# Kernel tuning notes

Hardware: AMD Instinct MI355X
Metric: run time of the kernel (lower is better)

Reference implementation:

```python
import jax, jax.numpy as jnp
import numpy as np

B, L, R, D = 64, 512, 512, 512
F_CONV, H = 100, 60

def setup_inputs() -> dict:
    key = jax.random.key(0)
    ks = jax.random.split(key, 8)
    l_lengths = jax.random.randint(ks[0], (B,), L // 2, L + 1)
    r_lengths = jax.random.randint(ks[1], (B,), R // 2, R + 1)
    l_vectors = jax.random.normal(ks[2], (L, B, D), jnp.float32)
    r_vectors = jax.random.normal(ks[3], (R, B, D), jnp.float32)
    Wconv = jax.random.normal(ks[4], (F_CONV, D), jnp.float32) / np.sqrt(D).astype(np.float32)
    bconv = jnp.zeros((F_CONV,), jnp.float32)
    Wd = jax.random.normal(ks[5], (H, 2 * F_CONV), jnp.float32) / np.sqrt(2 * F_CONV).astype(np.float32)
    bd = jnp.zeros((H,), jnp.float32)
    return {"l_lengths": l_lengths, "l_vectors": l_vectors, "r_lengths": r_lengths,
            "r_vectors": r_vectors, "Wconv": Wconv, "bconv": bconv, "Wd": Wd, "bd": bd}

def reference(l_lengths, l_vectors, r_lengths, r_vectors, Wconv, bconv, Wd, bd):
    Lm, Bm, Dm = l_vectors.shape
    Rm = r_vectors.shape[0]
    # masks, seq-first [L,B] like pad_sequence output
    l_mask = (jnp.arange(Lm)[:, None] < l_lengths[None, :]).astype(l_vectors.dtype)
    r_mask = (jnp.arange(Rm)[:, None] < r_lengths[None, :]).astype(r_vectors.dtype)
    lmT, rmT = l_mask.T, r_mask.T  # [B,L], [B,R]

    # co-attention scores [B,L,R]
    attention = jnp.einsum('lbd,rbd->blr', l_vectors, r_vectors)
    attention = attention * lmT[:, :, None] * rmT[:, None, :]

    att_r = jax.nn.softmax(attention - 10.0 * (1.0 - lmT[:, :, None]), axis=1)
    att_r = att_r * lmT[:, :, None]
    att_r = att_r / (att_r.sum(axis=1, keepdims=True) + 1e-13)

    att_l = jax.nn.softmax(attention - 10.0 * (1.0 - rmT[:, None, :]), axis=2)
    att_l = att_l * rmT[:, None, :]
    att_l = att_l / (att_l.sum(axis=2, keepdims=True) + 1e-13)

    # ---- left side: stats + top-1 hard attention ----
    rl = r_lengths.astype(l_vectors.dtype)[:, None]
    l_mean = att_l.sum(axis=2) / rl                              # [B,L]
    l_w = (att_l * att_l).sum(axis=2) / rl - l_mean * l_mean
    l_w = l_w / jnp.maximum(l_mean, 0.001)
    l_a = att_l.max(axis=2)                                      # top-1 value [B,L]
    l_i = att_l.argmax(axis=2)                                   # top-1 index [B,L]
    l_i = l_i * lmT.astype(l_i.dtype)
    l_a = l_a / jnp.maximum(l_a, 0.001)                          # k=1: sum == value
    gathered = jnp.take_along_axis(r_vectors, l_i.T[:, :, None], axis=0)  # [L,B,D]
    l_counter = l_a.T[:, :, None] * gathered
    l_c = l_w.T[:, :, None] * jnp.abs(l_vectors - l_counter) * l_mask[:, :, None]

    # ---- right side ----
    ll = l_lengths.astype(r_vectors.dtype)[:, None]
    r_mean = att_r.sum(axis=1) / ll                              # [B,R]
    r_w = (att_r * att_r).sum(axis=1) / ll - r_mean * r_mean
    r_w = r_w / jnp.maximum(r_mean, 0.001)
    r_a = att_r.max(axis=1)                                      # [B,R]
    r_i = att_r.argmax(axis=1)
    r_i = r_i * rmT.astype(r_i.dtype)
    r_a = r_a / jnp.maximum(r_a, 0.001)
    gathered_r = jnp.take_along_axis(l_vectors, r_i.T[:, :, None], axis=0)  # [R,B,D]
    r_counter = r_a.T[:, :, None] * gathered_r
    r_c = r_w.T[:, :, None] * jnp.abs(r_vectors - r_counter) * r_mask[:, :, None]

    # SentenceConv(1, 100, dim): kernel (1, dim) conv == per-position linear,
    # ReLU, masked max-pool over the sequence.
    def sconv(x, mask):  # x [S,B,D], mask [S,B]
        h = jax.nn.relu(jnp.einsum('sbd,fd->bsf', x, Wconv) + bconv)  # [B,S,F]
        h = h - (1.0 - mask.T)[:, :, None] * 1e9
        return h.max(axis=1)  # [B,F]

    feats = jnp.concatenate([sconv(l_c, l_mask), sconv(r_c, r_mask)], axis=1)  # [B,200]
    return jax.nn.relu(feats @ Wd.T + bd)  # [B,60]
```

## Files before the change

### kernel.cpp

```cpp
#include <hip/hip_runtime.h>
#include <math.h>

#define BB 64
#define LL 512
#define RR 512
#define DD 512
#define FC 100
#define FP 112
#define HH 60
#define BD (BB*DD)

typedef __attribute__((ext_vector_type(8))) short bf16x8;
typedef __attribute__((ext_vector_type(4))) float f32x4;

__device__ __forceinline__ unsigned short bf16rne(float x) {
  unsigned u = __float_as_uint(x);
  return (unsigned short)((u + 0x7fffu + ((u >> 16) & 1u)) >> 16);
}
__device__ __forceinline__ float bf16tof(unsigned short h) {
  return __uint_as_float((unsigned)h << 16);
}

__device__ __forceinline__ void bar_lgkm() {
  asm volatile("s_waitcnt lgkmcnt(0)" ::: "memory");
  __builtin_amdgcn_s_barrier();
}

__device__ __forceinline__ void split2(float x0, float x1, unsigned& h2, unsigned& l2) {
  unsigned u0 = __float_as_uint(x0), u1 = __float_as_uint(x1);
  h2 = __builtin_amdgcn_perm(u1, u0, 0x07060302u);
  float r0 = x0 - __uint_as_float(u0 & 0xffff0000u);
  float r1 = x1 - __uint_as_float(u1 & 0xffff0000u);
  l2 = __builtin_amdgcn_perm(__float_as_uint(r1), __float_as_uint(r0), 0x07060302u);
}

template <int N>
__device__ __forceinline__ float ror_max_f(float v) {
  return fmaxf(v, __uint_as_float(__builtin_amdgcn_mov_dpp(__float_as_uint(v), 0x120 | N, 0xf, 0xf, true)));
}
template <int N>
__device__ __forceinline__ float ror_add_f(float v) {
  return v + __uint_as_float(__builtin_amdgcn_mov_dpp(__float_as_uint(v), 0x120 | N, 0xf, 0xf, true));
}
template <int N>
__device__ __forceinline__ int ror_min_i(int v) {
  int o = __builtin_amdgcn_mov_dpp(v, 0x120 | N, 0xf, 0xf, true);
  return o < v ? o : v;
}
__device__ __forceinline__ float row16_max(float v) {
  v = ror_max_f<1>(v); v = ror_max_f<2>(v); v = ror_max_f<4>(v); return ror_max_f<8>(v);
}
__device__ __forceinline__ float row16_sum(float v) {
  v = ror_add_f<1>(v); v = ror_add_f<2>(v); v = ror_add_f<4>(v); return ror_add_f<8>(v);
}
__device__ __forceinline__ int row16_min(int v) {
  v = ror_min_i<1>(v); v = ror_min_i<2>(v); v = ror_min_i<4>(v); return ror_min_i<8>(v);
}

__global__ __launch_bounds__(512, 2) void gemm_att(const float* __restrict__ lv,
                                                   const float* __restrict__ rv,
                                                   const int* __restrict__ llen,
                                                   const int* __restrict__ rlen,
                                                   float4* __restrict__ lpart,
                                                   float4* __restrict__ rpart) {
  __shared__ __align__(16) unsigned short Ah[2][256][32];
  __shared__ __align__(16) unsigned short Al[2][256][32];
  __shared__ __align__(16) unsigned short Bh[2][256][32];
  __shared__ __align__(16) unsigned short Bl[2][256][32];

  const int bid = blockIdx.x;
  const int wid = (bid & 7) * 32 + (bid >> 3);
  const int b  = wid >> 2;
  const int l0 = ((wid >> 1) & 1) * 256;
  const int r0 = (wid & 1) * 256;

  const int t = threadIdx.x;
  const int srow = t >> 1;
  const int half = t & 1;

  const float* Abase = lv + (size_t)(l0 + srow) * BD + b * DD + half * 16;
  const float* Bbase = rv + (size_t)(r0 + srow) * BD + b * DD + half * 16;

  const int sl0 = (((2 * half) ^ ((srow >> 1) & 3)) * 8);
  const int sl1 = (((2 * half + 1) ^ ((srow >> 1) & 3)) * 8);

  const int lane = t & 63;
  const int wv = t >> 6;
  const int wrow = wv >> 2;
  const int wcol = wv & 3;
  const int fr = lane & 15;
  const int kh = lane >> 4;
  const int koff = (kh ^ ((fr >> 1) & 3)) * 8;

  float4 pa[4], pb[4];

#define LOADCHUNK(n) { const int cn_ = ((n) < 15 ? (n) : 15) * 32; \
    const float* An = Abase + cn_; const float* Bn = Bbase + cn_; \
    pa[0] = *(const float4*)(An);     pa[1] = *(const float4*)(An + 4); \
    pa[2] = *(const float4*)(An + 8); pa[3] = *(const float4*)(An + 12); \
    pb[0] = *(const float4*)(Bn);     pb[1] = *(const float4*)(Bn + 4); \
    pb[2] = *(const float4*)(Bn + 8); pb[3] = *(const float4*)(Bn + 12); }

#define STAGE(nb) { unsigned h01, l01, h23, l23, h45, l45, h67, l67; \
    split2(pa[0].x, pa[0].y, h01, l01); split2(pa[0].z, pa[0].w, h23, l23); \
    split2(pa[1].x, pa[1].y, h45, l45); split2(pa[1].z, pa[1].w, h67, l67); \
    *(uint4*)&Ah[nb][srow][sl0] = make_uint4(h01, h23, h45, h67); \
    *(uint4*)&Al[nb][srow][sl0] = make_uint4(l01, l23, l45, l67); \
    split2(pa[2].x, pa[2].y, h01, l01); split2(pa[2].z, pa[2].w, h23, l23); \
    split2(pa[3].x, pa[3].y, h45, l45); split2(pa[3].z, pa[3].w, h67, l67); \
    *(uint4*)&Ah[nb][srow][sl1] = make_uint4(h01, h23, h45, h67); \
    *(uint4*)&Al[nb][srow][sl1] = make_uint4(l01, l23, l45, l67); \
    split2(pb[0].x, pb[0].y, h01, l01); split2(pb[0].z, pb[0].w, h23, l23); \
    split2(pb[1].x, pb[1].y, h45, l45); split2(pb[1].z, pb[1].w, h67, l67); \
    *(uint4*)&Bh[nb][srow][sl0] = make_uint4(h01, h23, h45, h67); \
    *(uint4*)&Bl[nb][srow][sl0] = make_uint4(l01, l23, l45, l67); \
    split2(pb[2].x, pb[2].y, h01, l01); split2(pb[2].z, pb[2].w, h23, l23); \
    split2(pb[3].x, pb[3].y, h45, l45); split2(pb[3].z, pb[3].w, h67, l67); \
    *(uint4*)&Bh[nb][srow][sl1] = make_uint4(h01, h23, h45, h67); \
    *(uint4*)&Bl[nb][srow][sl1] = make_uint4(l01, l23, l45, l67); }

#define COMPUTE(cb) { bf16x8 bh4[4], bl4[4]; \
    _Pragma("unroll") \
    for (int j = 0; j < 4; ++j) { \
      bh4[j] = *(const bf16x8*)&Bh[cb][wcol * 64 + j * 16 + fr][koff]; \
      bl4[j] = *(const bf16x8*)&Bl[cb][wcol * 64 + j * 16 + fr][koff]; \
    } \
    __builtin_amdgcn_s_setprio(1); \
    _Pragma("unroll") \
    for (int i = 0; i < 8; ++i) { \
      bf16x8 a_h = *(const bf16x8*)&Ah[cb][wrow * 128 + i * 16 + fr][koff]; \
      bf16x8 a_l = *(const bf16x8*)&Al[cb][wrow * 128 + i * 16 + fr][koff]; \
      _Pragma("unroll") \
      for (int j = 0; j < 4; ++j) { \
        acc[i][j] = __builtin_amdgcn_mfma_f32_16x16x32_bf16(a_h, bh4[j], acc[i][j], 0, 0, 0); \
        acc[i][j] = __builtin_amdgcn_mfma_f32_16x16x32_bf16(a_h, bl4[j], acc[i][j], 0, 0, 0); \
        acc[i][j] = __builtin_amdgcn_mfma_f32_16x16x32_bf16(a_l, bh4[j], acc[i][j], 0, 0, 0); \
      } \
    } \
    __builtin_amdgcn_s_setprio(0); }

  f32x4 acc[8][4];
#pragma unroll
  for (int i = 0; i < 8; ++i)
#pragma unroll
    for (int j = 0; j < 4; ++j) acc[i][j] = (f32x4){0.f, 0.f, 0.f, 0.f};

  LOADCHUNK(0);
  STAGE(0);
  LOADCHUNK(1);
  bar_lgkm();

  for (int p2 = 0; p2 < 8; ++p2) {
    const int c = p2 * 2;
    STAGE(1);
    LOADCHUNK(c + 2);
    COMPUTE(0);
    bar_lgkm();
    STAGE(0);
    LOADCHUNK(c + 3);
    COMPUTE(1);
    bar_lgkm();
  }

  const int ll_ = llen[b], rl_ = rlen[b];
  __syncthreads();
  float4* rowsc = (float4*)&Ah[0][0][0];
  float4* colsc = (float4*)&Bh[0][0][0];

  const int rbase = r0 + wcol * 64 + fr;
  bool vr4[4]; int rr4[4];
#pragma unroll
  for (int j = 0; j < 4; ++j) { rr4[j] = rbase + j * 16; vr4[j] = rr4[j] < rl_; }

#pragma unroll
  for (int i = 0; i < 8; ++i) {
#pragma unroll
    for (int q = 0; q < 4; ++q) {
      const int trow = wrow * 128 + i * 16 + kh * 4 + q;
      const bool vl = (l0 + trow) < ll_;
      float s[4];
      float M = -1e30f;
#pragma unroll
      for (int j = 0; j < 4; ++j) {
        float raw = acc[i][j][q];
        s[j] = !vr4[j] ? -10.f : (vl ? raw : 0.f);
        M = fmaxf(M, s[j]);
      }
      M = row16_max(M);
      float zv = 0.f, q2 = 0.f;
      int loc = 0x7fffffff;
#pragma unroll
      for (int j = 0; j < 4; ++j) {
        float e = __expf(s[j] - M);
        if (vr4[j]) {
          zv += e; q2 += e * e;
          if (s[j] == M && rr4[j] < loc) loc = rr4[j];
        }
      }
      zv = row16_sum(zv);
      q2 = row16_sum(q2);
      loc = row16_min(loc);
      if (fr == 0)
        rowsc[wcol * 256 + trow] = make_float4(M, zv, q2, __int_as_float(loc));
    }
  }

#pragma unroll
  for (int j = 0; j < 4; ++j) {
    const int tcol = wcol * 64 + j * 16 + fr;
    const bool vr = (r0 + tcol) < rl_;
    float M = -1e30f;
#pragma unroll
    for (int i = 0; i < 8; ++i)
#pragma unroll
      for (int q = 0; q < 4; ++q) {
        int lg = l0 + wrow * 128 + i * 16 + kh * 4 + q;
        bool vl = lg < ll_;
        float sv = !vl ? -10.f : (vr ? acc[i][j][q] : 0.f);
        M = fmaxf(M, sv);
      }
    M = fmaxf(M, __shfl_xor(M, 16, 64));
    M = fmaxf(M, __shfl_xor(M, 32, 64));
    float zv = 0.f, q2 = 0.f;
    int loc = 0x7fffffff;
#pragma unroll
    for (int i = 0; i < 8; ++i)
#pragma unroll
      for (int q = 0; q < 4; ++q) {
        int lg = l0 + wrow * 128 + i * 16 + kh * 4 + q;
        bool vl = lg < ll_;
        float sv = !vl ? -10.f : (vr ? acc[i][j][q] : 0.f);
        float e = __expf(sv - M);
        if (vl) {
          zv += e; q2 += e * e;
          if (sv == M && lg < loc) loc = lg;
        }
      }
    zv += __shfl_xor(zv, 16, 64); zv += __shfl_xor(zv, 32, 64);
    q2 += __shfl_xor(q2, 16, 64); q2 += __shfl_xor(q2, 32, 64);
    { int o = __shfl_xor(loc, 16, 64); loc = o < loc ? o : loc; }
    { int o = __shfl_xor(loc, 32, 64); loc = o < loc ? o : loc; }
    if (kh == 0)
      colsc[wrow * 256 + tcol] = make_float4(M, zv, q2, __int_as_float(loc));
  }

  __syncthreads();

  if (t < 256) {
    float4 p = rowsc[t];
    float M = p.x, zv = p.y, q2 = p.z;
    int loc = __float_as_int(p.w);
#pragma unroll
    for (int w2 = 1; w2 < 4; ++w2) {
      float4 o = rowsc[w2 * 256 + t];
      float M1 = o.x;
      float Mn = fmaxf(M, M1);
      float c0 = __expf(M - Mn), c1 = __expf(M1 - Mn);
      zv = zv * c0 + o.y * c1;
      q2 = q2 * c0 * c0 + o.z * c1 * c1;
      int loc1 = __float_as_int(o.w);
      loc = (M1 > M) ? loc1 : ((M1 == M && loc1 < loc) ? loc1 : loc);
      M = Mn;
    }
    lpart[((size_t)(b * 512 + l0 + t)) * 2 + (r0 >> 8)] =
        make_float4(M, zv, q2, __int_as_float(loc));
  } else {
    const int c = t - 256;
    float4 p = colsc[c];
    float M = p.x, zv = p.y, q2 = p.z;
    int loc = __float_as_int(p.w);
    {
      float4 o = colsc[256 + c];
      float M1 = o.x;
      float Mn = fmaxf(M, M1);
      float c0 = __expf(M - Mn), c1 = __expf(M1 - Mn);
      zv = zv * c0 + o.y * c1;
      q2 = q2 * c0 * c0 + o.z * c1 * c1;
      int loc1 = __float_as_int(o.w);
      loc = (M1 > M) ? loc1 : ((M1 == M && loc1 < loc) ? loc1 : loc);
      M = Mn;
    }
    rpart[((size_t)(b * 512 + r0 + c)) * 2 + (l0 >> 8)] =
        make_float4(M, zv, q2, __int_as_float(loc));
  }
#undef LOADCHUNK
#undef STAGE
#undef COMPUTE
}

__global__ __launch_bounds__(256) void stats_merge(const float4* __restrict__ lpart,
    const float4* __restrict__ rpart,
    const int* __restrict__ llen, const int* __restrict__ rlen,
    float* __restrict__ lwv, float* __restrict__ lan, int* __restrict__ lidx,
    float* __restrict__ rwv, float* __restrict__ ran, int* __restrict__ ridx) {
  const int gid = blockIdx.x * 256 + threadIdx.x;
  const int side = gid >> 15;
  const int pos = gid & 32767;
  const int b = pos >> 9, p = pos & 511;
  const float4* part = (side ? rpart : lpart) + (size_t)pos * 2;
  float4 P0 = part[0], P1 = part[1];
  float M = P0.x, zv = P0.y, q2 = P0.z;
  int loc = __float_as_int(P0.w);
  {
    float M1 = P1.x;
    float Mn = fmaxf(M, M1);
    float c0 = __expf(M - Mn), c1 = __expf(M1 - Mn);
    zv = zv * c0 + P1.y * c1;
    q2 = q2 * c0 * c0 + P1.z * c1 * c1;
    int loc1 = __float_as_int(P1.w);
    loc = (M1 > M) ? loc1 : ((M1 == M && loc1 < loc) ? loc1 : loc);
    M = Mn;
  }
  const int len = side ? llen[b] : rlen[b];
  const int own = side ? rlen[b] : llen[b];
  const int ninv = side ? (LL - llen[b]) : (RR - rlen[b]);
  float z0 = zv + (float)ninv * __expf(-10.f - M);
  float S = zv / z0;
  float inv = 1.f / (S + 1e-13f);
  float sumq = S * inv;
  float mean = sumq / (float)len;
  float sumq2 = q2 / (z0 * z0) * inv * inv;
  float var = sumq2 / (float)len - mean * mean;
  float wv = var / fmaxf(mean, 0.001f);
  float qmax = inv / z0;
  float an = qmax / fmaxf(qmax, 0.001f);
  int idx = (p < own && loc != 0x7fffffff) ? loc : 0;
  if (side == 0) { lwv[pos] = wv; lan[pos] = an; lidx[pos] = idx; }
  else           { rwv[pos] = wv; ran[pos] = an; ridx[pos] = idx; }
}

__global__ void prep_w(const float* __restrict__ Wconv,
                       unsigned short* __restrict__ Whg, unsigned short* __restrict__ Wlg) {
  int i = blockIdx.x * 256 + threadIdx.x;
  if (i < FP * DD) {
    int f = i >> 9;
    float w = (f < FC) ? Wconv[i] : 0.f;
    unsigned short h = bf16rne(w);
    unsigned short l = bf16rne(w - bf16tof(h));
    Whg[i] = h; Wlg[i] = l;
  }
}

__global__ __launch_bounds__(256, 2) void conv_pool_mfma(const float* __restrict__ lv,
    const float* __restrict__ rv,
    const float* __restrict__ lwv, const float* __restrict__ lan, const int* __restrict__ lidx,
    const float* __restrict__ rwv, const float* __restrict__ ran, const int* __restrict__ ridx,
    const int* __restrict__ llen, const int* __restrict__ rlen,
    const unsigned short* __restrict__ Whg, const unsigned short* __restrict__ Wlg,
    const float* __restrict__ bconv, float* __restrict__ feat) {
  __shared__ __align__(16) unsigned short Ah[2][128][32];
  __shared__ __align__(16) unsigned short Al[2][128][32];
  __shared__ __align__(16) unsigned short Wh[2][FP][32];
  __shared__ __align__(16) unsigned short Wl[2][FP][32];
  __shared__ float pool[4][FP];
  __shared__ float ppw[128], ppa[128];
  __shared__ int   ppi[128], ppv[128];

  const int bid = blockIdx.x;
  const int wid = (bid & 7) * 64 + (bid >> 3);
  const int side = wid >> 8;
  const int b    = (wid >> 2) & 63;
  const int s0   = (wid & 3) * 128;

  const int t = threadIdx.x;
  const float* x; const float* y; const float* wb; const float* ab; const int* ib; int plen;
  if (side == 0) { x = lv; y = rv; wb = lwv; ab = lan; ib = lidx; plen = llen[b]; }
  else           { x = rv; y = lv; wb = rwv; ab = ran; ib = ridx; plen = rlen[b]; }

  if (t < 128) {
    int pos = s0 + t;
    ppw[t] = wb[b * 512 + pos];
    ppa[t] = ab[b * 512 + pos];
    ppi[t] = ib[b * 512 + pos];
    ppv[t] = (pos < plen) ? 1 : 0;
  }
  __syncthreads();

  const int pos  = t >> 1;
  const int half = t & 1;
  const float w_ = ppw[pos];
  const float a_ = ppa[pos];
  const int   yi = ppi[pos];
  const float* xp = x + (size_t)(s0 + pos) * BD + b * DD + half * 16;
  const float* yp = y + (size_t)yi * BD + b * DD + half * 16;

  const int asl0 = (((2 * half) ^ ((pos >> 1) & 3)) * 8);
  const int asl1 = (((2 * half + 1) ^ ((pos >> 1) & 3)) * 8);

  const int idx1 = (t < 192) ? t + 256 : t;
  const int f0 = t >> 2,   q0 = t & 3;
  const int f1 = idx1 >> 2, q1 = idx1 & 3;
  const int wsl0 = ((q0 ^ ((f0 >> 1) & 3)) * 8);
  const int wsl1 = ((q1 ^ ((f1 >> 1) & 3)) * 8);

  const int lane = t & 63;
  const int wvi = t >> 6;
  const int m0 = wvi * 32;
  const int fr = lane & 15;
  const int kh = lane >> 4;
  const int koff = (kh ^ ((fr >> 1) & 3)) * 8;

  float4 xv[4], yv[4];
  uint4 w0h, w0l, w1h, w1l;

#define LOADX(n) { const int off = ((n) < 15 ? (n) : 15) * 32; \
    xv[0] = *(const float4*)(xp + off);      xv[1] = *(const float4*)(xp + off + 4); \
    xv[2] = *(const float4*)(xp + off + 8);  xv[3] = *(const float4*)(xp + off + 12); \
    yv[0] = *(const float4*)(yp + off);      yv[1] = *(const float4*)(yp + off + 4); \
    yv[2] = *(const float4*)(yp + off + 8);  yv[3] = *(const float4*)(yp + off + 12); }

#define LOADW(n) { const int off = ((n) < 15 ? (n) : 15) * 32; \
    w0h = *(const uint4*)&Whg[f0 * DD + off + q0 * 8]; \
    w0l = *(const uint4*)&Wlg[f0 * DD + off + q0 * 8]; \
    w1h = *(const uint4*)&Whg[f1 * DD + off + q1 * 8]; \
    w1l = *(const uint4*)&Wlg[f1 * DD + off + q1 * 8]; }

#define STAGEA(nb) { \
    float d0 = w_ * fabsf(xv[0].x - a_ * yv[0].x); \
    float d1 = w_ * fabsf(xv[0].y - a_ * yv[0].y); \
    float d2 = w_ * fabsf(xv[0].z - a_ * yv[0].z); \
    float d3 = w_ * fabsf(xv[0].w - a_ * yv[0].w); \
    float d4 = w_ * fabsf(xv[1].x - a_ * yv[1].x); \
    float d5 = w_ * fabsf(xv[1].y - a_ * yv[1].y); \
    float d6 = w_ * fabsf(xv[1].z - a_ * yv[1].z); \
    float d7 = w_ * fabsf(xv[1].w - a_ * yv[1].w); \
    unsigned h01, l01, h23, l23, h45, l45, h67, l67; \
    split2(d0, d1, h01, l01); split2(d2, d3, h23, l23); \
    split2(d4, d5, h45, l45); split2(d6, d7, h67, l67); \
    *(uint4*)&Ah[nb][pos][asl0] = make_uint4(h01, h23, h45, h67); \
    *(uint4*)&Al[nb][pos][asl0] = make_uint4(l01, l23, l45, l67); \
    d0 = w_ * fabsf(xv[2].x - a_ * yv[2].x); \
    d1 = w_ * fabsf(xv[2].y - a_ * yv[2].y); \
    d2 = w_ * fabsf(xv[2].z - a_ * yv[2].z); \
    d3 = w_ * fabsf(xv[2].w - a_ * yv[2].w); \
    d4 = w_ * fabsf(xv[3].x - a_ * yv[3].x); \
    d5 = w_ * fabsf(xv[3].y - a_ * yv[3].y); \
    d6 = w_ * fabsf(xv[3].z - a_ * yv[3].z); \
    d7 = w_ * fabsf(xv[3].w - a_ * yv[3].w); \
    split2(d0, d1, h01, l01); split2(d2, d3, h23, l23); \
    split2(d4, d5, h45, l45); split2(d6, d7, h67, l67); \
    *(uint4*)&Ah[nb][pos][asl1] = make_uint4(h01, h23, h45, h67); \
    *(uint4*)&Al[nb][pos][asl1] = make_uint4(l01, l23, l45, l67); }

#define STAGEW(nb) { \
    *(uint4*)&Wh[nb][f0][wsl0] = w0h; *(uint4*)&Wl[nb][f0][wsl0] = w0l; \
    *(uint4*)&Wh[nb][f1][wsl1] = w1h; *(uint4*)&Wl[nb][f1][wsl1] = w1l; }

#define COMPUTEC(cb) { bf16x8 ah[2], al[2]; \
    _Pragma("unroll") \
    for (int i = 0; i < 2; ++i) { \
      ah[i] = *(const bf16x8*)&Ah[cb][m0 + i * 16 + fr][koff]; \
      al[i] = *(const bf16x8*)&Al[cb][m0 + i * 16 + fr][koff]; \
    } \
    __builtin_amdgcn_s_setprio(1); \
    _Pragma("unroll") \
    for (int j = 0; j < 7; ++j) { \
      bf16x8 bh = *(const bf16x8*)&Wh[cb][j * 16 + fr][koff]; \
      bf16x8 bl = *(const bf16x8*)&Wl[cb][j * 16 + fr][koff]; \
      _Pragma("unroll") \
      for (int i = 0; i < 2; ++i) { \
        acc[i][j] = __builtin_amdgcn_mfma_f32_16x16x32_bf16(ah[i], bh, acc[i][j], 0, 0, 0); \
        acc[i][j] = __builtin_amdgcn_mfma_f32_16x16x32_bf16(ah[i], bl, acc[i][j], 0, 0, 0); \
        acc[i][j] = __builtin_amdgcn_mfma_f32_16x16x32_bf16(al[i], bh, acc[i][j], 0, 0, 0); \
      } \
    } \
    __builtin_amdgcn_s_setprio(0); }

  f32x4 acc[2][7];
#pragma unroll
  for (int i = 0; i < 2; ++i)
#pragma unroll
    for (int j = 0; j < 7; ++j) acc[i][j] = (f32x4){0.f, 0.f, 0.f, 0.f};

  LOADX(0); LOADW(0);
  STAGEA(0); STAGEW(0);
  LOADX(1); LOADW(1);
  bar_lgkm();

  for (int p2 = 0; p2 < 8; ++p2) {
    const int c = p2 * 2;
    STAGEA(1); STAGEW(1);
    LOADX(c + 2); LOADW(c + 2);
    COMPUTEC(0);
    bar_lgkm();
    STAGEA(0); STAGEW(0);
    LOADX(c + 3); LOADW(c + 3);
    COMPUTEC(1);
    bar_lgkm();
  }

#pragma unroll
  for (int j = 0; j < 7; ++j) {
    int f = j * 16 + fr;
    float bcv = (f < FC) ? bconv[f] : 0.f;
    float vmax = -1e30f;
#pragma unroll
    for (int i = 0; i < 2; ++i) {
#pragma unroll
      for (int q = 0; q < 4; ++q) {
        int sl = m0 + i * 16 + kh * 4 + q;
        if (ppv[sl]) vmax = fmaxf(vmax, fmaxf(acc[i][j][q] + bcv, 0.f));
      }
    }
    vmax = fmaxf(vmax, __shfl_xor(vmax, 16, 64));
    vmax = fmaxf(vmax, __shfl_xor(vmax, 32, 64));
    if (lane < 16) pool[wvi][f] = vmax;
  }
  __syncthreads();
  if (t < FC) {
    float v = fmaxf(fmaxf(pool[0][t], pool[1][t]), fmaxf(pool[2][t], pool[3][t]));
    if (v > -1e29f) atomicMax((int*)&feat[b * 200 + side * FC + t], __float_as_int(v));
  }
#undef LOADX
#undef LOADW
#undef STAGEA
#undef STAGEW
#undef COMPUTEC
}

__global__ void dense_out(const float* __restrict__ feat, const float* __restrict__ Wd,
                          const float* __restrict__ bd, float* __restrict__ out) {
  int b = blockIdx.x, h = threadIdx.x;
  if (h < HH) {
    float s = bd[h];
    const float* fb = feat + b * 200;
    const float* wr = Wd + h * 200;
    for (int k = 0; k < 200; ++k) s += fb[k] * wr[k];
    out[b * HH + h] = fmaxf(s, 0.f);
  }
}

extern "C" void kernel_launch(void* const* d_in, const int* in_sizes, int n_in,
                              void* d_out, int out_size, void* d_ws, size_t ws_size,
                              hipStream_t stream) {
  (void)in_sizes; (void)n_in; (void)out_size; (void)ws_size;
  const int*   llen  = (const int*)d_in[0];
  const float* lv    = (const float*)d_in[1];
  const int*   rlen  = (const int*)d_in[2];
  const float* rv    = (const float*)d_in[3];
  const float* Wconv = (const float*)d_in[4];
  const float* bconv = (const float*)d_in[5];
  const float* Wd    = (const float*)d_in[6];
  const float* bd    = (const float*)d_in[7];
  float* out = (float*)d_out;
  char* ws = (char*)d_ws;
  size_t off = 0;
  unsigned short* Whg = (unsigned short*)(ws + off); off += (size_t)FP * DD * 2;
  unsigned short* Wlg = (unsigned short*)(ws + off); off += (size_t)FP * DD * 2;
  float4* lpart = (float4*)(ws + off); off += (size_t)BB * LL * 2 * 16;
  float4* rpart = (float4*)(ws + off); off += (size_t)BB * RR * 2 * 16;
  float* lwv = (float*)(ws + off); off += (size_t)BB * LL * 4;
  float* lan = (float*)(ws + off); off += (size_t)BB * LL * 4;
  int*   lidx= (int*)  (ws + off); off += (size_t)BB * LL * 4;
  float* rwv = (float*)(ws + off); off += (size_t)BB * RR * 4;
  float* ran = (float*)(ws + off); off += (size_t)BB * RR * 4;
  int*   ridx= (int*)  (ws + off); off += (size_t)BB * RR * 4;
  float* feat= (float*)(ws + off); off += (size_t)BB * 200 * 4;

  hipMemsetAsync(feat, 0, BB * 200 * 4, stream);
  prep_w<<<(FP * DD + 255) / 256, 256, 0, stream>>>(Wconv, Whg, Wlg);
  gemm_att<<<dim3(256), 512, 0, stream>>>(lv, rv, llen, rlen, lpart, rpart);
  stats_merge<<<dim3(256), 256, 0, stream>>>(lpart, rpart, llen, rlen,
                                             lwv, lan, lidx, rwv, ran, ridx);
  conv_pool_mfma<<<dim3(512), 256, 0, stream>>>(lv, rv, lwv, lan, lidx,
                                                rwv, ran, ridx, llen, rlen,
                                                Whg, Wlg, bconv, feat);
  dense_out<<<BB, 64, 0, stream>>>(feat, Wd, bd, out);
}
```

Measured before the change: 116.4 us.

## Fuse stats merge into conv kernel, drop atomics, split MFMA phase around staging

Folds the stats_merge kernel into the prologue of conv_pool_mfma, so each block recomputes its own row stats straight from the partial softmax buffers. This removes one launch and the round trip of the intermediate arrays through memory. Cross-block pooling now writes per-block partial maxima into a workspace that dense_out reduces, replacing the memset and the float atomicMax. The MFMA loop is also reordered: LDS staging and global loads for the next chunk sit between two halves of the compute, to overlap memory with matrix math.

Result: faster. 113.5 us (-2.5%).

```diff
diff --git a/kernel.cpp b/kernel.cpp
--- a/kernel.cpp
+++ b/kernel.cpp
@@ -288,47 +288,6 @@
 #undef COMPUTE
 }
 
-__global__ __launch_bounds__(256) void stats_merge(const float4* __restrict__ lpart,
-    const float4* __restrict__ rpart,
-    const int* __restrict__ llen, const int* __restrict__ rlen,
-    float* __restrict__ lwv, float* __restrict__ lan, int* __restrict__ lidx,
-    float* __restrict__ rwv, float* __restrict__ ran, int* __restrict__ ridx) {
-  const int gid = blockIdx.x * 256 + threadIdx.x;
-  const int side = gid >> 15;
-  const int pos = gid & 32767;
-  const int b = pos >> 9, p = pos & 511;
-  const float4* part = (side ? rpart : lpart) + (size_t)pos * 2;
-  float4 P0 = part[0], P1 = part[1];
-  float M = P0.x, zv = P0.y, q2 = P0.z;
-  int loc = __float_as_int(P0.w);
-  {
-    float M1 = P1.x;
-    float Mn = fmaxf(M, M1);
-    float c0 = __expf(M - Mn), c1 = __expf(M1 - Mn);
-    zv = zv * c0 + P1.y * c1;
-    q2 = q2 * c0 * c0 + P1.z * c1 * c1;
-    int loc1 = __float_as_int(P1.w);
-    loc = (M1 > M) ? loc1 : ((M1 == M && loc1 < loc) ? loc1 : loc);
-    M = Mn;
-  }
-  const int len = side ? llen[b] : rlen[b];
-  const int own = side ? rlen[b] : llen[b];
-  const int ninv = side ? (LL - llen[b]) : (RR - rlen[b]);
-  float z0 = zv + (float)ninv * __expf(-10.f - M);
-  float S = zv / z0;
-  float inv = 1.f / (S + 1e-13f);
-  float sumq = S * inv;
-  float mean = sumq / (float)len;
-  float sumq2 = q2 / (z0 * z0) * inv * inv;
-  float var = sumq2 / (float)len - mean * mean;
-  float wv = var / fmaxf(mean, 0.001f);
-  float qmax = inv / z0;
-  float an = qmax / fmaxf(qmax, 0.001f);
-  int idx = (p < own && loc != 0x7fffffff) ? loc : 0;
-  if (side == 0) { lwv[pos] = wv; lan[pos] = an; lidx[pos] = idx; }
-  else           { rwv[pos] = wv; ran[pos] = an; ridx[pos] = idx; }
-}
-
 __global__ void prep_w(const float* __restrict__ Wconv,
                        unsigned short* __restrict__ Whg, unsigned short* __restrict__ Wlg) {
   int i = blockIdx.x * 256 + threadIdx.x;
@@ -343,11 +302,10 @@
 
 __global__ __launch_bounds__(256, 2) void conv_pool_mfma(const float* __restrict__ lv,
     const float* __restrict__ rv,
-    const float* __restrict__ lwv, const float* __restrict__ lan, const int* __restrict__ lidx,
-    const float* __restrict__ rwv, const float* __restrict__ ran, const int* __restrict__ ridx,
+    const float4* __restrict__ lpart, const float4* __restrict__ rpart,
     const int* __restrict__ llen, const int* __restrict__ rlen,
     const unsigned short* __restrict__ Whg, const unsigned short* __restrict__ Wlg,
-    const float* __restrict__ bconv, float* __restrict__ feat) {
+    const float* __restrict__ bconv, float* __restrict__ poolws) {
   __shared__ __align__(16) unsigned short Ah[2][128][32];
   __shared__ __align__(16) unsigned short Al[2][128][32];
   __shared__ __align__(16) unsigned short Wh[2][FP][32];
@@ -363,15 +321,40 @@
   const int s0   = (wid & 3) * 128;
 
   const int t = threadIdx.x;
-  const float* x; const float* y; const float* wb; const float* ab; const int* ib; int plen;
-  if (side == 0) { x = lv; y = rv; wb = lwv; ab = lan; ib = lidx; plen = llen[b]; }
-  else           { x = rv; y = lv; wb = rwv; ab = ran; ib = ridx; plen = rlen[b]; }
+  const int ll_b = llen[b], rl_b = rlen[b];
+  const float* x; const float* y; int plen;
+  if (side == 0) { x = lv; y = rv; plen = ll_b; }
+  else           { x = rv; y = lv; plen = rl_b; }
 
   if (t < 128) {
     int pos = s0 + t;
-    ppw[t] = wb[b * 512 + pos];
-    ppa[t] = ab[b * 512 + pos];
-    ppi[t] = ib[b * 512 + pos];
+    const float4* part = (side ? rpart : lpart) + (size_t)(b * 512 + pos) * 2;
+    float4 P0 = part[0], P1 = part[1];
+    float M = P0.x, zv = P0.y, q2v = P0.z;
+    int loc = __float_as_int(P0.w);
+    {
+      float M1 = P1.x;
+      float Mn = fmaxf(M, M1);
+      float c0 = __expf(M - Mn), c1 = __expf(M1 - Mn);
+      zv = zv * c0 + P1.y * c1;
+      q2v = q2v * c0 * c0 + P1.z * c1 * c1;
+      int loc1 = __float_as_int(P1.w);
+      loc = (M1 > M) ? loc1 : ((M1 == M && loc1 < loc) ? loc1 : loc);
+      M = Mn;
+    }
+    const int len  = side ? ll_b : rl_b;
+    const int own  = side ? rl_b : ll_b;
+    const int ninv = side ? (LL - ll_b) : (RR - rl_b);
+    float z0 = zv + (float)ninv * __expf(-10.f - M);
+    float S = zv / z0;
+    float inv = 1.f / (S + 1e-13f);
+    float mean = S * inv / (float)len;
+    float sumq2 = q2v / (z0 * z0) * inv * inv;
+    float var = sumq2 / (float)len - mean * mean;
+    ppw[t] = var / fmaxf(mean, 0.001f);
+    float qmax = inv / z0;
+    ppa[t] = qmax / fmaxf(qmax, 0.001f);
+    ppi[t] = (pos < own && loc != 0x7fffffff) ? loc : 0;
     ppv[t] = (pos < plen) ? 1 : 0;
   }
   __syncthreads();
@@ -446,23 +429,37 @@
     *(uint4*)&Wh[nb][f0][wsl0] = w0h; *(uint4*)&Wl[nb][f0][wsl0] = w0l; \
     *(uint4*)&Wh[nb][f1][wsl1] = w1h; *(uint4*)&Wl[nb][f1][wsl1] = w1l; }
 
-#define COMPUTEC(cb) { bf16x8 ah[2], al[2]; \
-    _Pragma("unroll") \
-    for (int i = 0; i < 2; ++i) { \
-      ah[i] = *(const bf16x8*)&Ah[cb][m0 + i * 16 + fr][koff]; \
-      al[i] = *(const bf16x8*)&Al[cb][m0 + i * 16 + fr][koff]; \
-    } \
+#define PHASEC(cb, nb, n) { bf16x8 ah0, ah1, al0, al1; \
+    ah0 = *(const bf16x8*)&Ah[cb][m0 + fr][koff]; \
+    ah1 = *(const bf16x8*)&Ah[cb][m0 + 16 + fr][koff]; \
+    al0 = *(const bf16x8*)&Al[cb][m0 + fr][koff]; \
+    al1 = *(const bf16x8*)&Al[cb][m0 + 16 + fr][koff]; \
     __builtin_amdgcn_s_setprio(1); \
     _Pragma("unroll") \
-    for (int j = 0; j < 7; ++j) { \
+    for (int j = 0; j < 3; ++j) { \
       bf16x8 bh = *(const bf16x8*)&Wh[cb][j * 16 + fr][koff]; \
       bf16x8 bl = *(const bf16x8*)&Wl[cb][j * 16 + fr][koff]; \
-      _Pragma("unroll") \
-      for (int i = 0; i < 2; ++i) { \
-        acc[i][j] = __builtin_amdgcn_mfma_f32_16x16x32_bf16(ah[i], bh, acc[i][j], 0, 0, 0); \
-        acc[i][j] = __builtin_amdgcn_mfma_f32_16x16x32_bf16(ah[i], bl, acc[i][j], 0, 0, 0); \
-        acc[i][j] = __builtin_amdgcn_mfma_f32_16x16x32_bf16(al[i], bh, acc[i][j], 0, 0, 0); \
-      } \
+      acc[0][j] = __builtin_amdgcn_mfma_f32_16x16x32_bf16(ah0, bh, acc[0][j], 0, 0, 0); \
+      acc[0][j] = __builtin_amdgcn_mfma_f32_16x16x32_bf16(ah0, bl, acc[0][j], 0, 0, 0); \
+      acc[0][j] = __builtin_amdgcn_mfma_f32_16x16x32_bf16(al0, bh, acc[0][j], 0, 0, 0); \
+      acc[1][j] = __builtin_amdgcn_mfma_f32_16x16x32_bf16(ah1, bh, acc[1][j], 0, 0, 0); \
+      acc[1][j] = __builtin_amdgcn_mfma_f32_16x16x32_bf16(ah1, bl, acc[1][j], 0, 0, 0); \
+      acc[1][j] = __builtin_amdgcn_mfma_f32_16x16x32_bf16(al1, bh, acc[1][j], 0, 0, 0); \
+    } \
+    __builtin_amdgcn_s_setprio(0); \
+    STAGEA(nb); STAGEW(nb); \
+    LOADX(n); LOADW(n); \
+    __builtin_amdgcn_s_setprio(1); \
+    _Pragma("unroll") \
+    for (int j = 3; j < 7; ++j) { \
+      bf16x8 bh = *(const bf16x8*)&Wh[cb][j * 16 + fr][koff]; \
+      bf16x8 bl = *(const bf16x8*)&Wl[cb][j * 16 + fr][koff]; \
+      acc[0][j] = __builtin_amdgcn_mfma_f32_16x16x32_bf16(ah0, bh, acc[0][j], 0, 0, 0); \
+      acc[0][j] = __builtin_amdgcn_mfma_f32_16x16x32_bf16(ah0, bl, acc[0][j], 0, 0, 0); \
+      acc[0][j] = __builtin_amdgcn_mfma_f32_16x16x32_bf16(al0, bh, acc[0][j], 0, 0, 0); \
+      acc[1][j] = __builtin_amdgcn_mfma_f32_16x16x32_bf16(ah1, bh, acc[1][j], 0, 0, 0); \
+      acc[1][j] = __builtin_amdgcn_mfma_f32_16x16x32_bf16(ah1, bl, acc[1][j], 0, 0, 0); \
+      acc[1][j] = __builtin_amdgcn_mfma_f32_16x16x32_bf16(al1, bh, acc[1][j], 0, 0, 0); \
     } \
     __builtin_amdgcn_s_setprio(0); }
 
@@ -479,13 +476,9 @@
 
   for (int p2 = 0; p2 < 8; ++p2) {
     const int c = p2 * 2;
-    STAGEA(1); STAGEW(1);
-    LOADX(c + 2); LOADW(c + 2);
-    COMPUTEC(0);
+    PHASEC(0, 1, c + 2);
     bar_lgkm();
-    STAGEA(0); STAGEW(0);
-    LOADX(c + 3); LOADW(c + 3);
-    COMPUTEC(1);
+    PHASEC(1, 0, c + 3);
     bar_lgkm();
   }
 
@@ -509,24 +502,32 @@
   __syncthreads();
   if (t < FC) {
     float v = fmaxf(fmaxf(pool[0][t], pool[1][t]), fmaxf(pool[2][t], pool[3][t]));
-    if (v > -1e29f) atomicMax((int*)&feat[b * 200 + side * FC + t], __float_as_int(v));
+    poolws[(((size_t)side * 64 + b) * 4 + (wid & 3)) * FP + t] = v;
   }
 #undef LOADX
 #undef LOADW
 #undef STAGEA
 #undef STAGEW
-#undef COMPUTEC
-}
-
-__global__ void dense_out(const float* __restrict__ feat, const float* __restrict__ Wd,
+#undef PHASEC
+}
+
+__global__ __launch_bounds__(256) void dense_out(const float* __restrict__ poolws,
+                          const float* __restrict__ Wd,
                           const float* __restrict__ bd, float* __restrict__ out) {
-  int b = blockIdx.x, h = threadIdx.x;
-  if (h < HH) {
-    float s = bd[h];
-    const float* fb = feat + b * 200;
-    const float* wr = Wd + h * 200;
-    for (int k = 0; k < 200; ++k) s += fb[k] * wr[k];
-    out[b * HH + h] = fmaxf(s, 0.f);
+  __shared__ float fs[200];
+  const int b = blockIdx.x, t = threadIdx.x;
+  if (t < 200) {
+    int side = t / FC, f = t - side * FC;
+    const float* p = poolws + (((size_t)side * 64 + b) * 4) * FP + f;
+    float v = fmaxf(fmaxf(p[0], p[FP]), fmaxf(p[2 * FP], p[3 * FP]));
+    fs[t] = (v > -1e29f) ? v : 0.f;
+  }
+  __syncthreads();
+  if (t < HH) {
+    float s = bd[t];
+    const float* wr = Wd + t * 200;
+    for (int k = 0; k < 200; ++k) s += fs[k] * wr[k];
+    out[b * HH + t] = fmaxf(s, 0.f);
   }
 }
 
@@ -549,21 +550,11 @@
   unsigned short* Wlg = (unsigned short*)(ws + off); off += (size_t)FP * DD * 2;
   float4* lpart = (float4*)(ws + off); off += (size_t)BB * LL * 2 * 16;
   float4* rpart = (float4*)(ws + off); off += (size_t)BB * RR * 2 * 16;
-  float* lwv = (float*)(ws + off); off += (size_t)BB * LL * 4;
-  float* lan = (float*)(ws + off); off += (size_t)BB * LL * 4;
-  int*   lidx= (int*)  (ws + off); off += (size_t)BB * LL * 4;
-  float* rwv = (float*)(ws + off); off += (size_t)BB * RR * 4;
-  float* ran = (float*)(ws + off); off += (size_t)BB * RR * 4;
-  int*   ridx= (int*)  (ws + off); off += (size_t)BB * RR * 4;
-  float* feat= (float*)(ws + off); off += (size_t)BB * 200 * 4;
-
-  hipMemsetAsync(feat, 0, BB * 200 * 4, stream);
+  float* poolws = (float*)(ws + off); off += (size_t)2 * BB * 4 * FP * 4;
+
   prep_w<<<(FP * DD + 255) / 256, 256, 0, stream>>>(Wconv, Whg, Wlg);
   gemm_att<<<dim3(256), 512, 0, stream>>>(lv, rv, llen, rlen, lpart, rpart);
-  stats_merge<<<dim3(256), 256, 0, stream>>>(lpart, rpart, llen, rlen,
-                                             lwv, lan, lidx, rwv, ran, ridx);
-  conv_pool_mfma<<<dim3(512), 256, 0, stream>>>(lv, rv, lwv, lan, lidx,
-                                                rwv, ran, ridx, llen, rlen,
-                                                Whg, Wlg, bconv, feat);
-  dense_out<<<BB, 64, 0, stream>>>(feat, Wd, bd, out);
-}
+  conv_pool_mfma<<<dim3(512), 256, 0, stream>>>(lv, rv, lpart, rpart, llen, rlen,
+                                                Whg, Wlg, bconv, poolws);
+  dense_out<<<BB, 256, 0, stream>>>(poolws, Wd, bd, out);
+}
```
